# Performance work log

Measured on AMD Instinct MI355X. Metric: run time of the kernel, lower is better.

## Reference

```python
import jax, jax.numpy as jnp
import numpy as np

B, S, T = 4096, 512, 32


def setup_inputs() -> dict:
    key = jax.random.key(0)
    k1, k2, k3, k4, k5 = jax.random.split(key, 5)
    emissions = jax.random.normal(k1, (B, S, T), dtype=jnp.float32)
    tags = jax.random.randint(k2, (B, S), 0, T)
    mask = jnp.ones((B, S), dtype=bool)
    transitions = jax.random.normal(k3, (T, T), dtype=jnp.float32)
    start_transitions = jax.random.normal(k4, (T,), dtype=jnp.float32)
    end_transitions = jax.random.normal(k5, (T,), dtype=jnp.float32)
    return {
        "emissions": emissions,
        "tags": tags,
        "mask": mask,
        "transitions": transitions,
        "start_transitions": start_transitions,
        "end_transitions": end_transitions,
    }


def _score_sentence(emissions, tags, mask, transitions, start_transitions, end_transitions):
    # gold path score, fully vectorized over batch and time
    t0 = tags[:, 0]
    score = start_transitions[t0]
    score = score + jnp.take_along_axis(emissions[:, 0], t0[:, None], axis=1)[:, 0]
    maskf = mask[:, 1:].astype(emissions.dtype)  # [B, S-1]
    trans_sc = transitions[tags[:, :-1], tags[:, 1:]]  # [B, S-1]
    emit_sc = jnp.take_along_axis(emissions[:, 1:], tags[:, 1:, None], axis=2)[..., 0]
    score = score + ((trans_sc + emit_sc) * maskf).sum(axis=1)
    last_idx = mask.sum(axis=1).astype(jnp.int32) - 1  # [B]
    last_tags = jnp.take_along_axis(tags, last_idx[:, None], axis=1)[:, 0]
    score = score + end_transitions[last_tags]
    return score  # [B]


def _forward_algorithm(emissions, mask, transitions, start_transitions, end_transitions):
    # log partition via lax.scan over time; state is [B, T]
    score0 = start_transitions + emissions[:, 0]  # [B, T]
    em_rest = jnp.swapaxes(emissions[:, 1:], 0, 1)  # [S-1, B, T]
    mk_rest = jnp.swapaxes(mask[:, 1:], 0, 1)  # [S-1, B]

    def step(score, xs):
        em_i, m_i = xs
        # score[b,prev] + transitions[prev,next] + em_i[b,next]
        next_score = jax.nn.logsumexp(
            score[:, :, None] + transitions[None, :, :] + em_i[:, None, :], axis=1
        )
        score = jnp.where(m_i[:, None], next_score, score)
        return score, None

    score, _ = jax.lax.scan(step, score0, (em_rest, mk_rest))
    return jax.nn.logsumexp(score + end_transitions, axis=1)  # [B]


def reference(emissions, tags, mask, transitions, start_transitions, end_transitions):
    gold = _score_sentence(emissions, tags, mask, transitions, start_transitions, end_transitions)
    fwd = _forward_algorithm(emissions, mask, transitions, start_transitions, end_transitions)
    return (fwd - gold).mean()
```

## Files before the change

### kernel.cpp

```cpp
#include <hip/hip_runtime.h>


#define L2E 1.4426950408889634f
#define LN2 0.6931471805599453f
#define PD  16

typedef float v2f __attribute__((ext_vector_type(2)));

#define FMAC_ROR(N, acc, seed, cf) \
    asm("v_fmac_f32_dpp %0, %1, %2 row_ror:" #N " row_mask:0xf bank_mask:0xf" \
        : "+v"(acc) : "v"(seed), "v"(cf))
#define MUL_ROR(N, dst, seed, cf) \
    asm("v_mul_f32_dpp %0, %1, %2 row_ror:" #N " row_mask:0xf bank_mask:0xf" \
        : "=v"(dst) : "v"(seed), "v"(cf))
#define MIRROR_ROR(N, dst, src) \
    (dst) = __builtin_amdgcn_update_dpp(0, (src), 0x120 + (N), 0xf, 0xf, false)
#define EXP2_OPAQUE(dst, src) \
    asm("v_exp_f32 %0, %1\n\ts_nop 1" : "=v"(dst) : "v"(src))
#define SNOP_PIN(x) asm("s_nop 1" : "+v"(x))

__global__ __launch_bounds__(256, 2) void crf_kernel(
    const float* __restrict__ emissions,
    const int*   __restrict__ tags,
    const float* __restrict__ transitions,
    const float* __restrict__ start_t,
    const float* __restrict__ end_t,
    float* __restrict__ out)
{
    constexpr int S = 512, T = 32;

    __shared__ float trans_raw[T * T];
    __shared__ __align__(16) float u_lds[4][2][T];
    __shared__ float res_lds[8];

    const int tid  = threadIdx.x;
    const int lane = tid & 63;
    const int g    = (lane >> 5) & 1;
    const int r    = (lane >> 4) & 1;
    const int p    = lane & 15;
    const int c    = lane & 31;
    const int wv   = tid >> 6;
    const long b   = ((long)blockIdx.x * 4 + wv) * 2 + g;

    #pragma unroll
    for (int k = 0; k < 4; ++k)
        trans_raw[tid + 256 * k] = transitions[tid + 256 * k];
    __syncthreads();

    int pi[16];
    pi[0] = p;
    MIRROR_ROR( 1, pi[ 1], p);  MIRROR_ROR( 2, pi[ 2], p);
    MIRROR_ROR( 3, pi[ 3], p);  MIRROR_ROR( 4, pi[ 4], p);
    MIRROR_ROR( 5, pi[ 5], p);  MIRROR_ROR( 6, pi[ 6], p);
    MIRROR_ROR( 7, pi[ 7], p);  MIRROR_ROR( 8, pi[ 8], p);
    MIRROR_ROR( 9, pi[ 9], p);  MIRROR_ROR(10, pi[10], p);
    MIRROR_ROR(11, pi[11], p);  MIRROR_ROR(12, pi[12], p);
    MIRROR_ROR(13, pi[13], p);  MIRROR_ROR(14, pi[14], p);
    MIRROR_ROR(15, pi[15], p);

    float cfA[16], cfB[16];
    #pragma unroll
    for (int d = 0; d < 16; ++d) {
        float xa = trans_raw[(16 * r       + pi[d]) * T + c] * L2E;
        float xb = trans_raw[(16 * (r ^ 1) + d)     * T + c] * L2E;
        EXP2_OPAQUE(cfA[d], xa);
        EXP2_OPAQUE(cfB[d], xb);
    }
    v2f cfB2[8];
    #pragma unroll
    for (int h = 0; h < 8; ++h) cfB2[h] = (v2f){cfB[2 * h], cfB[2 * h + 1]};

    const float* em_base = emissions + b * (long)(S * T) + c;
    const int*   tg_base = tags + b * S;

    float em0      = em_base[0];
    int   tag_prev = tg_base[0];

    float em_buf[PD];
    int   tag_buf[PD];
    #pragma unroll
    for (int j = 0; j < PD; ++j) {
        em_buf[j]  = em_base[(long)(1 + j) * T];
        tag_buf[j] = tg_base[1 + j];
    }

    float startv = start_t[c];
    float u = __builtin_amdgcn_exp2f((startv + em0) * L2E);
    SNOP_PIN(u);
    int offs0 = 0, offs1 = 0;

    float gold_d = (c == tag_prev) ? (startv + em0) : 0.0f;
    float gold_u = 0.0f;

    float* u_row = &u_lds[wv][g][0];
    const float4* up = reinterpret_cast<const float4*>(&u_lds[wv][g][16 * (r ^ 1)]);

    auto step = [&](float em_cur, int tag_cur, bool rn) {
        float E = __builtin_amdgcn_exp2f(em_cur * L2E);
        if (rn) {
            unsigned e0 = (__builtin_amdgcn_readlane(__float_as_uint(u),  0))
                          & 0x7f800000u;
            unsigned e1 = (__builtin_amdgcn_readlane(__float_as_uint(u), 32))
                          & 0x7f800000u;
            offs0 += (int)(e0 >> 23) - 127;
            offs1 += (int)(e1 >> 23) - 127;
            unsigned sel = g ? e1 : e0;
            E *= __uint_as_float(0x7f000000u - sel);
        }

        u_row[c] = u;
        __builtin_amdgcn_wave_barrier();
        float4 w0 = up[0], w1 = up[1], w2 = up[2], w3 = up[3];
        __builtin_amdgcn_wave_barrier();

        float a0 = u * cfA[0];
        float a1, a2, a3;
        MUL_ROR ( 1, a1, u, cfA[ 1]);
        MUL_ROR ( 2, a2, u, cfA[ 2]);
        MUL_ROR ( 3, a3, u, cfA[ 3]);
        FMAC_ROR( 4, a0, u, cfA[ 4]);
        FMAC_ROR( 5, a1, u, cfA[ 5]);
        FMAC_ROR( 6, a2, u, cfA[ 6]);
        FMAC_ROR( 7, a3, u, cfA[ 7]);
        FMAC_ROR( 8, a0, u, cfA[ 8]);
        FMAC_ROR( 9, a1, u, cfA[ 9]);
        FMAC_ROR(10, a2, u, cfA[10]);
        FMAC_ROR(11, a3, u, cfA[11]);
        FMAC_ROR(12, a0, u, cfA[12]);
        FMAC_ROR(13, a1, u, cfA[13]);
        FMAC_ROR(14, a2, u, cfA[14]);
        FMAC_ROR(15, a3, u, cfA[15]);

        v2f p0 = (v2f){w0.x, w0.y} * cfB2[0];
        p0 = __builtin_elementwise_fma((v2f){w0.z, w0.w}, cfB2[1], p0);
        v2f p1 = (v2f){w1.x, w1.y} * cfB2[2];
        p1 = __builtin_elementwise_fma((v2f){w1.z, w1.w}, cfB2[3], p1);
        p0 = __builtin_elementwise_fma((v2f){w2.x, w2.y}, cfB2[4], p0);
        p1 = __builtin_elementwise_fma((v2f){w2.z, w2.w}, cfB2[5], p1);
        p0 = __builtin_elementwise_fma((v2f){w3.x, w3.y}, cfB2[6], p0);
        p1 = __builtin_elementwise_fma((v2f){w3.z, w3.w}, cfB2[7], p1);
        v2f q = p0 + p1;

        float dot = ((a0 + a1) + (a2 + a3)) + (q.x + q.y);
        u = dot * E;
        SNOP_PIN(u);

        gold_u += trans_raw[(tag_prev << 5) + tag_cur];
        gold_d += (c == tag_cur) ? em_cur : 0.0f;
        tag_prev = tag_cur;
    };

    for (int ii = 1; ii <= 465; ii += 16) {
        const float* pf_em = em_base + (long)(ii + 16) * T;
        const int*   pf_tg = tg_base + (ii + 16);
        #pragma unroll
        for (int j = 0; j < 16; ++j) {
            float em_cur = em_buf[j];
            int   tag_cur = tag_buf[j];
            em_buf[j]  = pf_em[(long)j * T];
            tag_buf[j] = pf_tg[j];
            step(em_cur, tag_cur, (j & 3) == 3);
        }
    }
    {
        const float* pf_em = em_base + (long)497 * T;
        const int*   pf_tg = tg_base + 497;
        #pragma unroll
        for (int j = 0; j < 15; ++j) {
            float em_cur = em_buf[j];
            int   tag_cur = tag_buf[j];
            em_buf[j]  = pf_em[(long)j * T];
            tag_buf[j] = pf_tg[j];
            step(em_cur, tag_cur, (j & 3) == 3);
        }
    }
    #pragma unroll
    for (int j = 0; j < 16; ++j) {
        const int bi = (j + 15) & 15;
        step(em_buf[bi], tag_buf[bi], (j & 3) == 0);
    }

    float endv = end_t[c];
    gold_d += (c == tag_prev) ? endv : 0.0f;

    float gd = gold_d;
    #pragma unroll
    for (int d = 16; d >= 1; d >>= 1) gd += __shfl_xor(gd, d, 64);
    float gold = gold_u + gd;

    float x = u * __builtin_amdgcn_exp2f(endv * L2E);
    float e = x;
    #pragma unroll
    for (int d = 16; d >= 1; d >>= 1) e += __shfl_xor(e, d, 64);
    float offsf = (float)(g ? offs1 : offs0);
    float fwd2  = offsf + __builtin_amdgcn_logf(e);

    float resv = fwd2 * LN2 - gold;

    if ((lane & 31) == 0) res_lds[wv * 2 + g] = resv;
    __syncthreads();
    if (tid == 0) {
        float ssum = 0.0f;
        #pragma unroll
        for (int q2 = 0; q2 < 8; ++q2) ssum += res_lds[q2];
        atomicAdd(out, ssum * (1.0f / 4096.0f));
    }
}

extern "C" void kernel_launch(void* const* d_in, const int* in_sizes, int n_in,
                              void* d_out, int out_size, void* d_ws, size_t ws_size,
                              hipStream_t stream) {
    const float* emissions   = (const float*)d_in[0];
    const int*   tags        = (const int*)d_in[1];
    const float* transitions = (const float*)d_in[3];
    const float* start_t     = (const float*)d_in[4];
    const float* end_t       = (const float*)d_in[5];
    float* out = (float*)d_out;

    hipMemsetAsync(out, 0, sizeof(float), stream);
    crf_kernel<<<512, 256, 0, stream>>>(emissions, tags, transitions,
                                        start_t, end_t, out);
}
```

Measured before the change: 399.1 us.

## Stage emissions through double-buffered LDS with float4 loads and lane-distributed tags

Replaces the per-lane scalar register prefetch of 16 emission rows and 16 tag values with wide float4 global loads into a double-buffered LDS tile. Each step reads its emission from LDS, and the tags are held one per lane and broadcast with readlane. The goal is to cut VGPR pressure from the 32-entry prefetch buffers and issue fewer, wider global loads. In exchange it adds LDS traffic and wave barriers to the serial recurrence, plus readlane latency on the critical path.

New measurement: 392.4 us. Within noise of the previous version (-1.7%).

```diff
diff --git a/kernel.cpp b/kernel.cpp
--- a/kernel.cpp
+++ b/kernel.cpp
@@ -3,7 +3,6 @@
 
 #define L2E 1.4426950408889634f
 #define LN2 0.6931471805599453f
-#define PD  16
 
 typedef float v2f __attribute__((ext_vector_type(2)));
 
@@ -31,6 +30,7 @@
 
     __shared__ float trans_raw[T * T];
     __shared__ __align__(16) float u_lds[4][2][T];
+    __shared__ __align__(16) float em_lds[4][2][2][16][T];
     __shared__ float res_lds[8];
 
     const int tid  = threadIdx.x;
@@ -41,6 +41,8 @@
     const int c    = lane & 31;
     const int wv   = tid >> 6;
     const long b   = ((long)blockIdx.x * 4 + wv) * 2 + g;
+    const int ls   = (lane >> 3) & 3;
+    const int lt   = lane & 7;
 
     #pragma unroll
     for (int k = 0; k < 4; ++k)
@@ -58,44 +60,68 @@
     MIRROR_ROR(13, pi[13], p);  MIRROR_ROR(14, pi[14], p);
     MIRROR_ROR(15, pi[15], p);
 
-    float cfA[16], cfB[16];
+    float cfA[16];
+    v2f cfB2[8];
     #pragma unroll
     for (int d = 0; d < 16; ++d) {
-        float xa = trans_raw[(16 * r       + pi[d]) * T + c] * L2E;
-        float xb = trans_raw[(16 * (r ^ 1) + d)     * T + c] * L2E;
+        float xa = trans_raw[(16 * r + pi[d]) * T + c] * L2E;
         EXP2_OPAQUE(cfA[d], xa);
-        EXP2_OPAQUE(cfB[d], xb);
-    }
-    v2f cfB2[8];
-    #pragma unroll
-    for (int h = 0; h < 8; ++h) cfB2[h] = (v2f){cfB[2 * h], cfB[2 * h + 1]};
+    }
+    #pragma unroll
+    for (int h = 0; h < 8; ++h) {
+        float x0 = trans_raw[(16 * (r ^ 1) + 2 * h)     * T + c] * L2E;
+        float x1 = trans_raw[(16 * (r ^ 1) + 2 * h + 1) * T + c] * L2E;
+        float c0, c1;
+        EXP2_OPAQUE(c0, x0);
+        EXP2_OPAQUE(c1, x1);
+        cfB2[h] = (v2f){c0, c1};
+    }
 
     const float* em_base = emissions + b * (long)(S * T) + c;
     const int*   tg_base = tags + b * S;
-
-    float em0      = em_base[0];
-    int   tag_prev = tg_base[0];
-
-    float em_buf[PD];
-    int   tag_buf[PD];
-    #pragma unroll
-    for (int j = 0; j < PD; ++j) {
-        em_buf[j]  = em_base[(long)(1 + j) * T];
-        tag_buf[j] = tg_base[1 + j];
-    }
+    const float* em_ld0  = emissions + b * (long)(S * T) + 4 * lt;
+
+    float em0     = em_base[0];
+    int   tp_lane = tg_base[0];
 
     float startv = start_t[c];
     float u = __builtin_amdgcn_exp2f((startv + em0) * L2E);
     SNOP_PIN(u);
     int offs0 = 0, offs1 = 0;
-
-    float gold_d = (c == tag_prev) ? (startv + em0) : 0.0f;
+    float gold_d = (c == tp_lane) ? (startv + em0) : 0.0f;
     float gold_u = 0.0f;
 
     float* u_row = &u_lds[wv][g][0];
     const float4* up = reinterpret_cast<const float4*>(&u_lds[wv][g][16 * (r ^ 1)]);
-
-    auto step = [&](float em_cur, int tag_cur, bool rn) {
+    float* emw       = &em_lds[wv][0][g][ls][4 * lt];
+    const float* emr = &em_lds[wv][0][g][0][c];
+
+    int tv_cur, tv_nxt;
+    float4 pc0, pc1, pc2, pc3;
+    {
+        tv_cur = tg_base[1 + (lane & 15)];
+        float4 q0 = *(const float4*)(em_ld0 + (long)( 1 + ls) * T);
+        float4 q1 = *(const float4*)(em_ld0 + (long)( 5 + ls) * T);
+        float4 q2 = *(const float4*)(em_ld0 + (long)( 9 + ls) * T);
+        float4 q3 = *(const float4*)(em_ld0 + (long)(13 + ls) * T);
+        tv_nxt = tg_base[17 + (lane & 15)];
+        pc0 = *(const float4*)(em_ld0 + (long)(17 + ls) * T);
+        pc1 = *(const float4*)(em_ld0 + (long)(21 + ls) * T);
+        pc2 = *(const float4*)(em_ld0 + (long)(25 + ls) * T);
+        pc3 = *(const float4*)(em_ld0 + (long)(29 + ls) * T);
+        *(float4*)(emw +   0) = q0;
+        *(float4*)(emw + 128) = q1;
+        *(float4*)(emw + 256) = q2;
+        *(float4*)(emw + 384) = q3;
+        __builtin_amdgcn_wave_barrier();
+    }
+
+    auto step = [&](int j, bool rn, const float* emr_c, int tvc) {
+        float em_cur = emr_c[j * 32];
+        int sA = __builtin_amdgcn_readlane(tvc, j);
+        int sB = __builtin_amdgcn_readlane(tvc, 32 + j);
+        int tc_lane = g ? sB : sA;
+
         float E = __builtin_amdgcn_exp2f(em_cur * L2E);
         if (rn) {
             unsigned e0 = (__builtin_amdgcn_readlane(__float_as_uint(u),  0))
@@ -139,49 +165,66 @@
         p1 = __builtin_elementwise_fma((v2f){w2.z, w2.w}, cfB2[5], p1);
         p0 = __builtin_elementwise_fma((v2f){w3.x, w3.y}, cfB2[6], p0);
         p1 = __builtin_elementwise_fma((v2f){w3.z, w3.w}, cfB2[7], p1);
-        v2f q = p0 + p1;
-
-        float dot = ((a0 + a1) + (a2 + a3)) + (q.x + q.y);
+        v2f qv = p0 + p1;
+
+        float dot = ((a0 + a1) + (a2 + a3)) + (qv.x + qv.y);
         u = dot * E;
         SNOP_PIN(u);
 
-        gold_u += trans_raw[(tag_prev << 5) + tag_cur];
-        gold_d += (c == tag_cur) ? em_cur : 0.0f;
-        tag_prev = tag_cur;
+        gold_u += trans_raw[(tp_lane << 5) + tc_lane];
+        gold_d += (c == tc_lane) ? em_cur : 0.0f;
+        tp_lane = tc_lane;
     };
 
-    for (int ii = 1; ii <= 465; ii += 16) {
-        const float* pf_em = em_base + (long)(ii + 16) * T;
-        const int*   pf_tg = tg_base + (ii + 16);
-        #pragma unroll
-        for (int j = 0; j < 16; ++j) {
-            float em_cur = em_buf[j];
-            int   tag_cur = tag_buf[j];
-            em_buf[j]  = pf_em[(long)j * T];
-            tag_buf[j] = pf_tg[j];
-            step(em_cur, tag_cur, (j & 3) == 3);
-        }
-    }
+    for (int k = 0; k <= 29; ++k) {
+        const int i0n = 16 * k + 33;
+        int idx = i0n + (lane & 15); if (idx > 511) idx = 511;
+        int tv_new = tg_base[idx];
+        int s0 = i0n +      ls; if (s0 > 511) s0 = 511;
+        int s1 = i0n +  4 + ls; if (s1 > 511) s1 = 511;
+        int s2 = i0n +  8 + ls; if (s2 > 511) s2 = 511;
+        int s3 = i0n + 12 + ls; if (s3 > 511) s3 = 511;
+        float4 pn0 = *(const float4*)(em_ld0 + (long)s0 * T);
+        float4 pn1 = *(const float4*)(em_ld0 + (long)s1 * T);
+        float4 pn2 = *(const float4*)(em_ld0 + (long)s2 * T);
+        float4 pn3 = *(const float4*)(em_ld0 + (long)s3 * T);
+
+        const float* emr_c = emr + (k & 1) * 1024;
+        #pragma unroll
+        for (int j = 0; j < 16; ++j)
+            step(j, (j & 3) == 3, emr_c, tv_cur);
+
+        float* emw_n = emw + ((k + 1) & 1) * 1024;
+        *(float4*)(emw_n +   0) = pc0;
+        *(float4*)(emw_n + 128) = pc1;
+        *(float4*)(emw_n + 256) = pc2;
+        *(float4*)(emw_n + 384) = pc3;
+        __builtin_amdgcn_wave_barrier();
+        pc0 = pn0; pc1 = pn1; pc2 = pn2; pc3 = pn3;
+        tv_cur = tv_nxt; tv_nxt = tv_new;
+    }
+
     {
-        const float* pf_em = em_base + (long)497 * T;
-        const int*   pf_tg = tg_base + 497;
-        #pragma unroll
-        for (int j = 0; j < 15; ++j) {
-            float em_cur = em_buf[j];
-            int   tag_cur = tag_buf[j];
-            em_buf[j]  = pf_em[(long)j * T];
-            tag_buf[j] = pf_tg[j];
-            step(em_cur, tag_cur, (j & 3) == 3);
-        }
-    }
-    #pragma unroll
-    for (int j = 0; j < 16; ++j) {
-        const int bi = (j + 15) & 15;
-        step(em_buf[bi], tag_buf[bi], (j & 3) == 0);
+        #pragma unroll
+        for (int j = 0; j < 16; ++j)
+            step(j, (j & 3) == 3, emr, tv_cur);
+        float* emw_n = emw + 1024;
+        *(float4*)(emw_n +   0) = pc0;
+        *(float4*)(emw_n + 128) = pc1;
+        *(float4*)(emw_n + 256) = pc2;
+        *(float4*)(emw_n + 384) = pc3;
+        __builtin_amdgcn_wave_barrier();
+        tv_cur = tv_nxt;
+    }
+    {
+        const float* emr_c = emr + 1024;
+        #pragma unroll
+        for (int j = 0; j < 15; ++j)
+            step(j, (j & 3) == 3, emr_c, tv_cur);
     }
 
     float endv = end_t[c];
-    gold_d += (c == tag_prev) ? endv : 0.0f;
+    gold_d += (c == tp_lane) ? endv : 0.0f;
 
     float gd = gold_d;
     #pragma unroll
```
